# Kernel optimization log

Measured on AMD Instinct MI355X. Metric: run time of the kernel, lower is better.

## Reference

```python
import jax, jax.numpy as jnp
import numpy as np
from jax import lax

B_, T_, C_ = 8, 1024, 768
H_, W_ = 32, 32
N_LAYER, LAYER_ID = 12, 5


def _fancy_init():
    # faithful 'fancy' init from Random_SpatialMix._init_weights
    r01 = LAYER_ID / (N_LAYER - 1)
    r1a0 = 1.0 - LAYER_ID / N_LAYER
    h = np.arange(C_, dtype=np.float64)
    decay = -5 + 8 * (h / (C_ - 1)) ** (0.7 + 1.3 * r01)
    zig = ((np.arange(C_) + 1) % 3 - 1) * 0.5
    first = np.log(0.3) + zig
    xlin = h / C_
    mix_k = xlin ** r1a0
    mix_v = xlin ** r1a0 + 0.3 * r01
    mix_r = xlin ** (0.5 * r1a0)
    f32 = lambda a: jnp.asarray(a, jnp.float32)
    return f32(decay), f32(first), f32(mix_k), f32(mix_v), f32(mix_r)


def setup_inputs() -> dict:
    key = jax.random.key(0)
    ks = jax.random.split(key, 6)
    s = 1.0 / np.sqrt(C_)
    x = jax.random.normal(ks[0], (B_, T_, C_), jnp.float32)
    Wk = jax.random.normal(ks[1], (C_, C_), jnp.float32) * s
    Wv = jax.random.normal(ks[2], (C_, C_), jnp.float32) * s
    Wr = jax.random.normal(ks[3], (C_, C_), jnp.float32) * s
    Wo = jax.random.normal(ks[4], (C_, C_), jnp.float32) * s
    decay, first, mk, mv, mr = _fancy_init()
    perm = jax.random.permutation(ks[5], C_).astype(jnp.int32)
    return dict(x=x, w_key=Wk, w_value=Wv, w_receptance=Wr, w_output=Wo,
                spatial_decay=decay, spatial_first=first,
                mix_k=mk, mix_v=mv, mix_r=mr, perm=perm, H=H_, W=W_)


def _shift2d(a, dh, dw, H, W):
    # zero-padded 2D shift of [B,H,W,g]
    pad = [(0, 0), (max(dh, 0), max(-dh, 0)), (max(dw, 0), max(-dw, 0)), (0, 0)]
    a = jnp.pad(a, pad)
    return a[:, max(-dh, 0):max(-dh, 0) + H, max(-dw, 0):max(-dw, 0) + W, :]


def q_shift(x, H, W, shift_pixel=1, gamma=0.25):
    # VRWKV q_shift: 4 channel groups shifted right/left/down/up, rest copied
    B, T, C = x.shape
    xi = x.reshape(B, H, W, C)
    g = int(C * gamma)
    parts = [
        _shift2d(xi[..., 0:g], 0, shift_pixel, H, W),
        _shift2d(xi[..., g:2 * g], 0, -shift_pixel, H, W),
        _shift2d(xi[..., 2 * g:3 * g], shift_pixel, 0, H, W),
        _shift2d(xi[..., 3 * g:4 * g], -shift_pixel, 0, H, W),
        xi[..., 4 * g:],
    ]
    return jnp.concatenate(parts, axis=-1).reshape(B, T, C)


def wkv(w, u, k, v):
    # RWKV-v4 WKV kernel (numerically stable form). w,u: [C]; k,v: [B,T,C]
    w = -jnp.exp(w)  # kernel applies w = -exp(w)
    B, T, C = k.shape

    def step(carry, kv):
        a, b, p = carry  # each [B,C]
        kt, vt = kv
        q = jnp.maximum(p, u + kt)
        e1 = jnp.exp(p - q)
        e2 = jnp.exp(u + kt - q)
        y = (e1 * a + e2 * vt) / (e1 * b + e2)
        q2 = jnp.maximum(p + w, kt)
        e1 = jnp.exp(p + w - q2)
        e2 = jnp.exp(kt - q2)
        return (e1 * a + e2 * vt, e1 * b + e2, q2), y

    init = (jnp.zeros((B, C), k.dtype), jnp.zeros((B, C), k.dtype),
            jnp.full((B, C), -1e38, k.dtype))
    _, y = lax.scan(step, init, (jnp.moveaxis(k, 1, 0), jnp.moveaxis(v, 1, 0)))
    return jnp.moveaxis(y, 0, 1)


def reference(x, w_key, w_value, w_receptance, w_output,
              spatial_decay, spatial_first, mix_k, mix_v, mix_r, perm, H, W):
    B, T, C = x.shape
    xx = q_shift(x, H, W)
    xk = x * mix_k + xx * (1 - mix_k)
    xv = x * mix_v + xx * (1 - mix_v)
    xr = x * mix_r + xx * (1 - mix_r)
    k = xk @ w_key.T
    v = xv @ w_value.T
    sr = jax.nn.sigmoid(xr @ w_receptance.T)
    # training path: shuffle CHANNEL axis (RevShuffle dim=2), run WKV, reverse
    ks_ = k[:, :, perm]
    vs_ = v[:, :, perm]
    wkv_s = wkv(spatial_decay / T, spatial_first / T, ks_, vs_)
    rev = jnp.zeros_like(perm).at[perm].set(jnp.arange(C, dtype=perm.dtype))
    wkv_out = wkv_s[:, :, rev]
    return (sr * wkv_out) @ w_output.T
```

## Files before the change

kernel.cpp:

```cpp
#include <hip/hip_runtime.h>
#include <hip/hip_bf16.h>
#include <stdint.h>

#define B_N 8
#define T_N 1024
#define C_N 768
#define M_N (B_N*T_N)
#define NCH 32
#define LCH (T_N/NCH)
#define BK32 32
#define KS  (C_N/BK32)

typedef __attribute__((ext_vector_type(4))) float f32x4;
typedef __attribute__((ext_vector_type(8))) short s16x8;
typedef __attribute__((ext_vector_type(4))) unsigned short u16x4;

__device__ __forceinline__ unsigned short f2bf(float f){
  unsigned int u = __float_as_uint(f);
  u += 0x7FFFu + ((u >> 16) & 1u);
  return (unsigned short)(u >> 16);
}
__device__ __forceinline__ float bf2f(unsigned short h){
  return __uint_as_float(((unsigned int)h) << 16);
}

__device__ __forceinline__ void async16(const unsigned short* g, unsigned short* l){
  __builtin_amdgcn_global_load_lds(
      (const __attribute__((address_space(1))) unsigned int*)g,
      (__attribute__((address_space(3))) unsigned int*)l, 16, 0, 0);
}

__global__ __launch_bounds__(256) void prep_mix(
    const float* __restrict__ x,
    const float* __restrict__ Wk, const float* __restrict__ Wv,
    const float* __restrict__ Wr, const float* __restrict__ Wo,
    const int* __restrict__ perm,
    const float* __restrict__ mk, const float* __restrict__ mv, const float* __restrict__ mr,
    unsigned short* __restrict__ Wall, unsigned short* __restrict__ Wop,
    unsigned short* __restrict__ xk, unsigned short* __restrict__ xv,
    unsigned short* __restrict__ xr)
{
  if (blockIdx.x < 2304){
    int idx = blockIdx.x*256 + threadIdx.x;
    int r = idx / C_N, c = idx - r*C_N;
    int pr = perm[r];
    Wall[idx]                     = f2bf(Wk[pr*C_N + c]);
    Wall[idx +   (size_t)C_N*C_N] = f2bf(Wv[pr*C_N + c]);
    Wall[idx + 2*(size_t)C_N*C_N] = f2bf(Wr[pr*C_N + c]);
    Wop[idx] = f2bf(Wo[r*C_N + perm[c]]);
    return;
  }
  int idx = (blockIdx.x - 2304)*256 + threadIdx.x;
  int n  = idx / (C_N/4);
  int c4 = (idx - n*(C_N/4)) * 4;
  int t = n & (T_N-1);
  int h = t >> 5, w = t & 31;
  int grp = c4 / 192;
  int dh = (grp==2) ? -1 : (grp==3) ? 1 : 0;
  int dw = (grp==0) ? -1 : (grp==1) ? 1 : 0;
  int h2 = h + dh, w2 = w + dw;
  bool valid = ((unsigned)h2 < 32u) && ((unsigned)w2 < 32u);
  f32x4 xc = *(const f32x4*)(x + (size_t)n*C_N + c4);
  f32x4 xx = {0.f,0.f,0.f,0.f};
  if (valid) xx = *(const f32x4*)(x + (size_t)(n + dh*32 + dw)*C_N + c4);
  f32x4 vk = *(const f32x4*)(mk + c4);
  f32x4 vv = *(const f32x4*)(mv + c4);
  f32x4 vr = *(const f32x4*)(mr + c4);
  u16x4 ok, ov, orr;
  #pragma unroll
  for (int i=0;i<4;++i){
    float d = xc[i] - xx[i];
    ok[i]  = f2bf(xx[i] + vk[i]*d);
    ov[i]  = f2bf(xx[i] + vv[i]*d);
    orr[i] = f2bf(xx[i] + vr[i]*d);
  }
  *(u16x4*)(xk + (size_t)n*C_N + c4) = ok;
  *(u16x4*)(xv + (size_t)n*C_N + c4) = ov;
  *(u16x4*)(xr + (size_t)n*C_N + c4) = orr;
}

__global__ __launch_bounds__(256, 3) void gemm_kvr(
    const unsigned short* __restrict__ xk, const unsigned short* __restrict__ xv,
    const unsigned short* __restrict__ xr,
    const unsigned short* __restrict__ Wall,
    unsigned short* __restrict__ kb, unsigned short* __restrict__ vb,
    unsigned short* __restrict__ srb)
{
  int flat = blockIdx.y * gridDim.x + blockIdx.x;
  const int xcd = flat & 7, q = flat >> 3;
  const int mb = xcd*8 + (q & 7);
  const int nb = q >> 3;
  const int m0 = mb * 128;
  const int n0 = nb * 128;
  const int z  = nb / 6;
  const unsigned short* A = (z==0)? xk : (z==1)? xv : xr;

  __shared__ union {
    struct { unsigned short As[3][128*BK32]; unsigned short Bs[3][128*BK32]; } s;
    unsigned short ct[128*132];
  } u;
  const int tid = threadIdx.x;
  const int lane = tid & 63, wid = tid >> 6;
  const int wr = wid >> 1, wc = wid & 1;
  f32x4 acc[4][4];
  #pragma unroll
  for (int i=0;i<4;++i)
    #pragma unroll
    for (int j=0;j<4;++j) acc[i][j] = (f32x4){0.f,0.f,0.f,0.f};

  const int sgcol = ((lane & 3) ^ ((lane >> 3) & 3)) * 8;
  const int srow  = lane >> 2;
  const int lr  = lane & 15;
  const int kh  = lane >> 4;
  const int phys = (kh ^ ((lr >> 1) & 3)) * 8;

  auto stage = [&](int buf, int k0){
    #pragma unroll
    for (int i=0;i<2;++i){
      int rbase = i*64 + wid*16;
      async16(&A   [(size_t)(m0 + rbase + srow)*C_N + k0 + sgcol], &u.s.As[buf][rbase*BK32]);
      async16(&Wall[(size_t)(n0 + rbase + srow)*C_N + k0 + sgcol], &u.s.Bs[buf][rbase*BK32]);
    }
  };

  auto compute = [&](int buf){
    s16x8 af[4], bfr[4];
    #pragma unroll
    for (int mi=0;mi<4;++mi) af[mi]  = *(const s16x8*)&u.s.As[buf][(wr*64 + mi*16 + lr)*BK32 + phys];
    #pragma unroll
    for (int ni=0;ni<4;++ni) bfr[ni] = *(const s16x8*)&u.s.Bs[buf][(wc*64 + ni*16 + lr)*BK32 + phys];
    __builtin_amdgcn_s_setprio(1);
    #pragma unroll
    for (int mi=0;mi<4;++mi)
      #pragma unroll
      for (int ni=0;ni<4;++ni)
        acc[mi][ni] = __builtin_amdgcn_mfma_f32_16x16x32_bf16(af[mi], bfr[ni], acc[mi][ni], 0,0,0);
    __builtin_amdgcn_s_setprio(0);
  };

  stage(0, 0);
  stage(1, BK32);
  #pragma unroll 1
  for (int t = 0; t < KS; ++t){
    if (t + 2 < KS) stage((t+2)%3, (t+2)*BK32);
    if (t + 2 < KS)      asm volatile("s_waitcnt vmcnt(8)" ::: "memory");
    else if (t + 1 < KS) asm volatile("s_waitcnt vmcnt(4)" ::: "memory");
    else                 asm volatile("s_waitcnt vmcnt(0)" ::: "memory");
    __builtin_amdgcn_s_barrier();
    compute(t%3);
    __builtin_amdgcn_s_barrier();
  }

  unsigned short* dst = (z==0)? kb : (z==1)? vb : srb;
  const int colbase = n0 - z*C_N;
  const int lr4 = (lane>>4)*4, lc = lane & 15;
  #pragma unroll
  for (int mi=0;mi<4;++mi){
    #pragma unroll
    for (int ni=0;ni<4;++ni){
      #pragma unroll
      for (int i=0;i<4;++i){
        int r  = wr*64 + mi*16 + lr4 + i;
        int cc = wc*64 + ni*16 + lc;
        float val = acc[mi][ni][i];
        if (z==2) val = 1.f/(1.f + __expf(-val));
        u.ct[r*132 + cc] = f2bf(val);
      }
    }
  }
  __builtin_amdgcn_s_barrier();
  #pragma unroll
  for (int p=0;p<8;++p){
    int f = (p*256 + tid)*8;
    int r = f >> 7, cc = f & 127;
    s16x8 v8 = *(const s16x8*)&u.ct[r*132 + cc];
    *(s16x8*)&dst[(size_t)(m0+r)*C_N + colbase + cc] = v8;
  }
}

__global__ __launch_bounds__(256, 3) void gemm_out(
    const unsigned short* __restrict__ A, const unsigned short* __restrict__ Bw,
    float* __restrict__ out)
{
  int flat = blockIdx.y * gridDim.x + blockIdx.x;
  const int xcd = flat & 7, q = flat >> 3;
  const int mb = xcd*8 + (q & 7);
  const int nb = q >> 3;
  const int m0 = mb*128, n0 = nb*128;
  __shared__ __align__(16) unsigned short As[3][128*BK32];
  __shared__ __align__(16) unsigned short Bs[3][128*BK32];
  const int tid = threadIdx.x;
  const int lane = tid & 63, wid = tid >> 6;
  const int wr = wid >> 1, wc = wid & 1;
  f32x4 acc[4][4];
  #pragma unroll
  for (int i=0;i<4;++i)
    #pragma unroll
    for (int j=0;j<4;++j) acc[i][j] = (f32x4){0.f,0.f,0.f,0.f};

  const int sgcol = ((lane & 3) ^ ((lane >> 3) & 3)) * 8;
  const int srow  = lane >> 2;
  const int lr  = lane & 15;
  const int kh  = lane >> 4;
  const int phys = (kh ^ ((lr >> 1) & 3)) * 8;

  auto stage = [&](int buf, int k0){
    #pragma unroll
    for (int i=0;i<2;++i){
      int rbase = i*64 + wid*16;
      async16(&A [(size_t)(m0 + rbase + srow)*C_N + k0 + sgcol], &As[buf][rbase*BK32]);
      async16(&Bw[(size_t)(n0 + rbase + srow)*C_N + k0 + sgcol], &Bs[buf][rbase*BK32]);
    }
  };

  auto compute = [&](int buf){
    s16x8 af[4], bfr[4];
    #pragma unroll
    for (int mi=0;mi<4;++mi) af[mi]  = *(const s16x8*)&As[buf][(wr*64 + mi*16 + lr)*BK32 + phys];
    #pragma unroll
    for (int ni=0;ni<4;++ni) bfr[ni] = *(const s16x8*)&Bs[buf][(wc*64 + ni*16 + lr)*BK32 + phys];
    __builtin_amdgcn_s_setprio(1);
    #pragma unroll
    for (int mi=0;mi<4;++mi)
      #pragma unroll
      for (int ni=0;ni<4;++ni)
        acc[mi][ni] = __builtin_amdgcn_mfma_f32_16x16x32_bf16(af[mi], bfr[ni], acc[mi][ni], 0,0,0);
    __builtin_amdgcn_s_setprio(0);
  };

  stage(0, 0);
  stage(1, BK32);
  #pragma unroll 1
  for (int t = 0; t < KS; ++t){
    if (t + 2 < KS) stage((t+2)%3, (t+2)*BK32);
    if (t + 2 < KS)      asm volatile("s_waitcnt vmcnt(8)" ::: "memory");
    else if (t + 1 < KS) asm volatile("s_waitcnt vmcnt(4)" ::: "memory");
    else                 asm volatile("s_waitcnt vmcnt(0)" ::: "memory");
    __builtin_amdgcn_s_barrier();
    compute(t%3);
    __builtin_amdgcn_s_barrier();
  }

  const int lr4 = (lane>>4)*4, lc = lane & 15;
  #pragma unroll
  for (int mi=0;mi<4;++mi)
    #pragma unroll
    for (int ni=0;ni<4;++ni)
      #pragma unroll
      for (int i=0;i<4;++i){
        int m = m0 + wr*64 + mi*16 + lr4 + i;
        int n = n0 + wc*64 + ni*16 + lc;
        out[(size_t)m*C_N + n] = acc[mi][ni][i];
      }
}

__global__ __launch_bounds__(256) void wkv_phase1(
    const unsigned short* __restrict__ kb, const unsigned short* __restrict__ vb,
    const float* __restrict__ decay,
    float* __restrict__ sa, float* __restrict__ sb, float* __restrict__ sp)
{
  int g = blockIdx.x*256 + threadIdx.x;
  int j = g % C_N;
  int cb = g / C_N;
  int b = cb % B_N, c = cb / B_N;
  float w = -__expf(decay[j] * (1.0f/T_N));
  float a = 0.f, bb = 0.f, p = -1e38f;
  size_t base = ((size_t)b*T_N + c*LCH)*C_N + j;
  #pragma unroll 4
  for (int t = 0; t < LCH; ++t){
    size_t o = base + (size_t)t*C_N;
    float kt = bf2f(kb[o]), vt = bf2f(vb[o]);
    float pw = p + w;
    float q2 = fmaxf(pw, kt);
    float e1 = __expf(pw - q2), e2 = __expf(kt - q2);
    a  = e1*a + e2*vt;
    bb = e1*bb + e2;
    p  = q2;
  }
  sa[g] = a; sb[g] = bb; sp[g] = p;
}

__global__ __launch_bounds__(256) void wkv_phase2(
    const float* __restrict__ decay,
    float* __restrict__ sa, float* __restrict__ sb, float* __restrict__ sp)
{
  int g = blockIdx.x*256 + threadIdx.x;
  int j = g % C_N, b = g / C_N;
  float w = -__expf(decay[j] * (1.0f/T_N));
  float wL = w * (float)LCH;
  float a = 0.f, bb = 0.f, p = -1e38f;
  for (int c = 0; c < NCH; ++c){
    size_t idx = ((size_t)c*B_N + b)*C_N + j;
    float la = sa[idx], lb = sb[idx], lp = sp[idx];
    sa[idx] = a; sb[idx] = bb; sp[idx] = p;
    float p1 = p + wL;
    float pn = fmaxf(p1, lp);
    float e1 = __expf(p1 - pn), e2 = __expf(lp - pn);
    a  = e1*a + e2*la;
    bb = e1*bb + e2*lb;
    p  = pn;
  }
}

__global__ __launch_bounds__(256) void wkv_phase3(
    const unsigned short* __restrict__ kb, const unsigned short* __restrict__ vb,
    const unsigned short* __restrict__ srb,
    const float* __restrict__ decay, const float* __restrict__ first,
    const float* __restrict__ sa, const float* __restrict__ sb,
    const float* __restrict__ sp,
    unsigned short* __restrict__ zp)
{
  int g = blockIdx.x*256 + threadIdx.x;
  int j = g % C_N;
  int cb = g / C_N;
  int b = cb % B_N, c = cb / B_N;
  float w = -__expf(decay[j] * (1.0f/T_N));
  float u = first[j] * (1.0f/T_N);
  float a = sa[g], bb = sb[g], p = sp[g];
  size_t base = ((size_t)b*T_N + c*LCH)*C_N + j;
  #pragma unroll 2
  for (int t = 0; t < LCH; ++t){
    size_t o = base + (size_t)t*C_N;
    float kt = bf2f(kb[o]), vt = bf2f(vb[o]);
    float uk = u + kt;
    float q  = fmaxf(p, uk);
    float e1 = __expf(p - q), e2 = __expf(uk - q);
    float y  = __fdividef(e1*a + e2*vt, e1*bb + e2);
    zp[o] = f2bf(bf2f(srb[o]) * y);
    float pw = p + w;
    float q2 = fmaxf(pw, kt);
    float e1b = __expf(pw - q2), e2b = __expf(kt - q2);
    a  = e1b*a + e2b*vt;
    bb = e1b*bb + e2b;
    p  = q2;
  }
}

extern "C" void kernel_launch(void* const* d_in, const int* in_sizes, int n_in,
                              void* d_out, int out_size, void* d_ws, size_t ws_size,
                              hipStream_t stream)
{
  const float* x     = (const float*)d_in[0];
  const float* Wk    = (const float*)d_in[1];
  const float* Wv    = (const float*)d_in[2];
  const float* Wr    = (const float*)d_in[3];
  const float* Wo    = (const float*)d_in[4];
  const float* decay = (const float*)d_in[5];
  const float* first = (const float*)d_in[6];
  const float* mk    = (const float*)d_in[7];
  const float* mv    = (const float*)d_in[8];
  const float* mr    = (const float*)d_in[9];
  const int*   perm  = (const int*)d_in[10];
  float* out = (float*)d_out;

  char* ws = (char*)d_ws;
  size_t off = 0;
  auto alloc = [&](size_t bytes)->char* {
    char* p = ws + off;
    off += (bytes + 255) & ~(size_t)255;
    return p;
  };
  const size_t MC = (size_t)M_N * C_N;
  const size_t CC = (size_t)C_N * C_N;
  const size_t SC = (size_t)NCH * B_N * C_N;
  unsigned short* xk   = (unsigned short*)alloc(MC*2);
  unsigned short* xv   = (unsigned short*)alloc(MC*2);
  unsigned short* xr   = (unsigned short*)alloc(MC*2);
  unsigned short* zp   = (unsigned short*)alloc(MC*2);
  unsigned short* Wall = (unsigned short*)alloc(CC*3*2);
  unsigned short* Wop  = (unsigned short*)alloc(CC*2);
  unsigned short* srb  = (unsigned short*)alloc(MC*2);
  unsigned short* kb   = (unsigned short*)alloc(MC*2);
  unsigned short* vb   = (unsigned short*)alloc(MC*2);
  float* sa  = (float*)alloc(SC*4);
  float* sb  = (float*)alloc(SC*4);
  float* sp  = (float*)alloc(SC*4);

  prep_mix<<<dim3(2304 + 6144), dim3(256), 0, stream>>>(
      x, Wk, Wv, Wr, Wo, perm, mk, mv, mr, Wall, Wop, xk, xv, xr);
  gemm_kvr<<<dim3(M_N/128, 3*C_N/128), dim3(256), 0, stream>>>(
      xk, xv, xr, Wall, kb, vb, srb);
  wkv_phase1<<<dim3(SC/256), dim3(256), 0, stream>>>(kb, vb, decay, sa, sb, sp);
  wkv_phase2<<<dim3(B_N*C_N/256), dim3(256), 0, stream>>>(decay, sa, sb, sp);
  wkv_phase3<<<dim3(SC/256), dim3(256), 0, stream>>>(kb, vb, srb, decay, first,
                                                     sa, sb, sp, zp);
  gemm_out<<<dim3(M_N/128, C_N/128), dim3(256), 0, stream>>>(zp, Wop, out);
}
```

Before: 109.7 us.

## Cut GEMM LDS to double buffering for four blocks per CU

```diff
diff --git a/kernel.cpp b/kernel.cpp
--- a/kernel.cpp
+++ b/kernel.cpp
@@ -79,7 +79,7 @@
   *(u16x4*)(xr + (size_t)n*C_N + c4) = orr;
 }
 
-__global__ __launch_bounds__(256, 3) void gemm_kvr(
+__global__ __launch_bounds__(256, 4) void gemm_kvr(
     const unsigned short* __restrict__ xk, const unsigned short* __restrict__ xv,
     const unsigned short* __restrict__ xr,
     const unsigned short* __restrict__ Wall,
@@ -96,8 +96,8 @@
   const unsigned short* A = (z==0)? xk : (z==1)? xv : xr;
 
   __shared__ union {
-    struct { unsigned short As[3][128*BK32]; unsigned short Bs[3][128*BK32]; } s;
-    unsigned short ct[128*132];
+    struct { unsigned short As[2][128*BK32]; unsigned short Bs[2][128*BK32]; } s;
+    unsigned short ct[64*132];
   } u;
   const int tid = threadIdx.x;
   const int lane = tid & 63, wid = tid >> 6;
@@ -139,15 +139,16 @@
   };
 
   stage(0, 0);
-  stage(1, BK32);
   #pragma unroll 1
   for (int t = 0; t < KS; ++t){
-    if (t + 2 < KS) stage((t+2)%3, (t+2)*BK32);
-    if (t + 2 < KS)      asm volatile("s_waitcnt vmcnt(8)" ::: "memory");
-    else if (t + 1 < KS) asm volatile("s_waitcnt vmcnt(4)" ::: "memory");
-    else                 asm volatile("s_waitcnt vmcnt(0)" ::: "memory");
-    __builtin_amdgcn_s_barrier();
-    compute(t%3);
+    if (t + 1 < KS){
+      stage((t+1)&1, (t+1)*BK32);
+      asm volatile("s_waitcnt vmcnt(4)" ::: "memory");
+    } else {
+      asm volatile("s_waitcnt vmcnt(0)" ::: "memory");
+    }
+    __builtin_amdgcn_s_barrier();
+    compute(t & 1);
     __builtin_amdgcn_s_barrier();
   }
 
@@ -155,30 +156,36 @@
   const int colbase = n0 - z*C_N;
   const int lr4 = (lane>>4)*4, lc = lane & 15;
   #pragma unroll
-  for (int mi=0;mi<4;++mi){
-    #pragma unroll
-    for (int ni=0;ni<4;++ni){
+  for (int p=0;p<2;++p){
+    if (p) __builtin_amdgcn_s_barrier();
+    if (wr == p){
       #pragma unroll
-      for (int i=0;i<4;++i){
-        int r  = wr*64 + mi*16 + lr4 + i;
-        int cc = wc*64 + ni*16 + lc;
-        float val = acc[mi][ni][i];
-        if (z==2) val = 1.f/(1.f + __expf(-val));
-        u.ct[r*132 + cc] = f2bf(val);
+      for (int mi=0;mi<4;++mi){
+        #pragma unroll
+        for (int ni=0;ni<4;++ni){
+          #pragma unroll
+          for (int i=0;i<4;++i){
+            int r  = mi*16 + lr4 + i;
+            int cc = wc*64 + ni*16 + lc;
+            float val = acc[mi][ni][i];
+            if (z==2) val = 1.f/(1.f + __expf(-val));
+            u.ct[r*132 + cc] = f2bf(val);
+          }
+        }
       }
     }
-  }
-  __builtin_amdgcn_s_barrier();
-  #pragma unroll
-  for (int p=0;p<8;++p){
-    int f = (p*256 + tid)*8;
-    int r = f >> 7, cc = f & 127;
-    s16x8 v8 = *(const s16x8*)&u.ct[r*132 + cc];
-    *(s16x8*)&dst[(size_t)(m0+r)*C_N + colbase + cc] = v8;
-  }
-}
-
-__global__ __launch_bounds__(256, 3) void gemm_out(
+    __builtin_amdgcn_s_barrier();
+    #pragma unroll
+    for (int qq=0;qq<4;++qq){
+      int f = (qq*256 + tid)*8;
+      int r = f >> 7, cc = f & 127;
+      s16x8 v8 = *(const s16x8*)&u.ct[r*132 + cc];
+      *(s16x8*)&dst[(size_t)(m0 + p*64 + r)*C_N + colbase + cc] = v8;
+    }
+  }
+}
+
+__global__ __launch_bounds__(256, 4) void gemm_out(
     const unsigned short* __restrict__ A, const unsigned short* __restrict__ Bw,
     float* __restrict__ out)
 {
@@ -187,8 +194,8 @@
   const int mb = xcd*8 + (q & 7);
   const int nb = q >> 3;
   const int m0 = mb*128, n0 = nb*128;
-  __shared__ __align__(16) unsigned short As[3][128*BK32];
-  __shared__ __align__(16) unsigned short Bs[3][128*BK32];
+  __shared__ __align__(16) unsigned short As[2][128*BK32];
+  __shared__ __align__(16) unsigned short Bs[2][128*BK32];
   const int tid = threadIdx.x;
   const int lane = tid & 63, wid = tid >> 6;
   const int wr = wid >> 1, wc = wid & 1;
@@ -229,15 +236,16 @@
   };
 
   stage(0, 0);
-  stage(1, BK32);
   #pragma unroll 1
   for (int t = 0; t < KS; ++t){
-    if (t + 2 < KS) stage((t+2)%3, (t+2)*BK32);
-    if (t + 2 < KS)      asm volatile("s_waitcnt vmcnt(8)" ::: "memory");
-    else if (t + 1 < KS) asm volatile("s_waitcnt vmcnt(4)" ::: "memory");
-    else                 asm volatile("s_waitcnt vmcnt(0)" ::: "memory");
-    __builtin_amdgcn_s_barrier();
-    compute(t%3);
+    if (t + 1 < KS){
+      stage((t+1)&1, (t+1)*BK32);
+      asm volatile("s_waitcnt vmcnt(4)" ::: "memory");
+    } else {
+      asm volatile("s_waitcnt vmcnt(0)" ::: "memory");
+    }
+    __builtin_amdgcn_s_barrier();
+    compute(t & 1);
     __builtin_amdgcn_s_barrier();
   }
 
```

New measurement: 113.7 us. +3.6%, slower.
